# Kernel optimization log

Hardware: AMD Instinct MI355X
Metric: run time of the kernel (lower is better)

## Reference

```python
import jax, jax.numpy as jnp
import numpy as np
from jax import lax

# Topology constants (windowed DAG: compute node i, at global index N_IN+i,
# reads the FANIN immediately preceding global node values).
N_IN = 16      # number of input nodes
FANIN = 16     # connections per compute node
N_NODES = 512  # topologically ordered compute nodes (hidden + output)
N_OUT = 64     # last N_OUT nodes in node_order are outputs
BATCH = 32768
T = N_IN + N_NODES  # total node count


def setup_inputs() -> dict:
    key = jax.random.key(0)
    k1, k2, k3, k4 = jax.random.split(key, 4)
    x = jax.random.normal(k1, (BATCH, N_IN), dtype=jnp.float32)
    # weights scaled down so tanh is not fully saturated through 512 layers
    weights = jax.random.normal(k2, (N_NODES, FANIN), dtype=jnp.float32) * 0.25
    biases = jax.random.normal(k3, (N_NODES,), dtype=jnp.float32) * 0.1
    responses = 1.0 + 0.1 * jax.random.normal(k4, (N_NODES,), dtype=jnp.float32)
    # src indices for node i: global indices [i, i+FANIN) (== previous FANIN nodes,
    # since N_IN == FANIN). Shape [N_NODES, FANIN], int32, all in [0, T).
    src_idx = (jnp.arange(N_NODES, dtype=jnp.int32)[:, None]
               + jnp.arange(FANIN, dtype=jnp.int32)[None, :]
               + (N_IN - FANIN))
    return {"x": x, "weights": weights, "biases": biases,
            "responses": responses, "src_idx": src_idx}


def _forward(x, weights, biases, responses, src_idx):
    B = x.shape[0]
    # values buffer [B, T]: inputs first, then compute nodes in topo order
    values0 = jnp.zeros((B, T), dtype=x.dtype).at[:, :N_IN].set(x)

    def body(values, xs):
        i, idx_row, w, b, r = xs
        src_vals = jnp.take(values, idx_row, axis=1)        # [B, FANIN] gather
        agg = src_vals @ w                                   # [B] weighted sum
        out = jnp.tanh(agg + b) * r                          # activation
        values = lax.dynamic_update_slice(values, out[:, None], (0, N_IN + i))
        return values, None

    ii = jnp.arange(N_NODES, dtype=jnp.int32)
    values, _ = lax.scan(body, values0, (ii, src_idx, weights, biases, responses))
    return values[:, T - N_OUT:]  # [B, N_OUT]


def reference(x, weights, biases, responses, src_idx):
    return _forward(x, weights, biases, responses, src_idx)
```

## Files before the change

### kernel.cpp

```cpp
#include <hip/hip_runtime.h>


typedef float    v4f __attribute__((ext_vector_type(4)));
typedef _Float16 h8  __attribute__((ext_vector_type(8)));

constexpr int   kNOut   = 64;
constexpr int   kBatch  = 32768;
constexpr int   kSgF    = 96;
constexpr int   kSgB    = 384;
constexpr int   kLdsFloats = 65 * kSgF;
constexpr float kScale  = 2.8853900817779268f;

#define QPERM(X, CTRL) __int_as_float(__builtin_amdgcn_update_dpp(            \
    __float_as_int(X), __float_as_int(X), (CTRL), 0xF, 0xF, false))

__device__ __forceinline__ unsigned pack2(float lo, float hi) {
    _Float16 l = (_Float16)lo, h = (_Float16)hi;
    unsigned short ul = __builtin_bit_cast(unsigned short, l);
    unsigned short uh = __builtin_bit_cast(unsigned short, h);
    return ((unsigned)uh << 16) | ul;
}

#define PREF(S) {                                                             \
    asm volatile(                                                             \
      "ds_read_b128 %0, %6 offset:0\n\t"                                      \
      "ds_read_b128 %1, %6 offset:64\n\t"                                     \
      "ds_read_b128 %2, %6 offset:128\n\t"                                    \
      "ds_read_b128 %3, %6 offset:192\n\t"                                    \
      "ds_read_b128 %4, %6 offset:256\n\t"                                    \
      "ds_read_b128 %5, %6 offset:320"                                        \
      : "=&v"(qw0[S]), "=&v"(qw1[S]), "=&v"(qw2[S]), "=&v"(qw3[S]),           \
        "=&v"(qm0[S]), "=&v"(qm1[S])                                          \
      : "v"(a));                                                              \
    a += kSgB; }

#define WAITR(S)                                                              \
    asm volatile("s_waitcnt lgkmcnt(6)"                                       \
      : "+v"(qw0[S]), "+v"(qw1[S]), "+v"(qw2[S]), "+v"(qw3[S]),               \
        "+v"(qm0[S]), "+v"(qm1[S]));

#define NODE(WPAIR, H, BQ, A0,A1,A2,A3) {                                     \
    h8 wh = __builtin_bit_cast(h8, (WPAIR));                                  \
    float p = fmaf((A0), (float)wh[4*(H)+0], (BQ));                           \
    p = fmaf((A1), (float)wh[4*(H)+1], p);                                    \
    p = fmaf((A2), (float)wh[4*(H)+2], p);                                    \
    p = fmaf((A3), (float)wh[4*(H)+3], p);                                    \
    float s1 = p + QPERM(p, 0xB1);                   \
    float s2 = s1 + QPERM(s1, 0x4E);                 \
    float mg = QPERM((A0), 0x39);                    \
    float ex = __builtin_amdgcn_exp2f(s2);                                    \
    float un = __builtin_amdgcn_rcpf(ex + 1.0f);                              \
    (A0) = is_l3 ? un : mg; }

#define REGION(SP, SC) {                                                      \
    PREF(SP)                                                                  \
    WAITR(SC)                                                                 \
    NODE(qw0[SC], 0, qm0[SC].x, r0,r1,r2,r3)                                  \
    NODE(qw0[SC], 1, qm0[SC].y, r1,r2,r3,r0)                                  \
    NODE(qw1[SC], 0, qm0[SC].z, r2,r3,r0,r1)                                  \
    NODE(qw1[SC], 1, qm0[SC].w, r3,r0,r1,r2)                                  \
    NODE(qw2[SC], 0, qm1[SC].x, r0,r1,r2,r3)                                  \
    NODE(qw2[SC], 1, qm1[SC].y, r1,r2,r3,r0)                                  \
    NODE(qw3[SC], 0, qm1[SC].z, r2,r3,r0,r1)                                  \
    NODE(qw3[SC], 1, qm1[SC].w, r3,r0,r1,r2) }

__global__ __launch_bounds__(512) void neat_fwd(
    const float* __restrict__ x,
    const float* __restrict__ w,
    const float* __restrict__ bias,
    const float* __restrict__ resp,
    float* __restrict__ out)
{
    __shared__ alignas(16) float ldsw[kLdsFloats];
    __shared__ float rst[512];

    const int t  = threadIdx.x;
    const int jq = t & 3;
    const bool is_l3 = (jq == 3);

    rst[t] = resp[t];
    __syncthreads();

    {
        const int n = t;
        const float4* wn = reinterpret_cast<const float4*>(w) + n * 4;
        float4 a0 = wn[0], a1 = wn[1], a2 = wn[2], a3 = wn[3];
        const float m2k = -2.0f * kScale;
        float sum = 0.0f;
        float ws0,ws1,ws2,ws3,ws4,ws5,ws6,ws7,ws8,ws9,ws10,ws11,ws12,ws13,ws14,ws15;
        #define DO(J, V) { float rho = (n + (J) < 16) ? 1.0f : rst[n + (J) - 16]; \
                           float wr = (V) * rho; sum += wr; ws##J = wr * m2k; }
        DO(0,a0.x)  DO(1,a0.y)  DO(2,a0.z)  DO(3,a0.w)
        DO(4,a1.x)  DO(5,a1.y)  DO(6,a1.z)  DO(7,a1.w)
        DO(8,a2.x)  DO(9,a2.y)  DO(10,a2.z) DO(11,a2.w)
        DO(12,a3.x) DO(13,a3.y) DO(14,a3.z) DO(15,a3.w)
        #undef DO
        const int sg = n >> 3, s = n & 7, m = s >> 1, h = s & 1;
        unsigned* lu = reinterpret_cast<unsigned*>(ldsw);
        int wi = sg * 96 + m * 16 + h * 2;
        lu[wi + 0*4 + 0] = pack2(ws0,  ws1);   lu[wi + 0*4 + 1] = pack2(ws2,  ws3);
        lu[wi + 1*4 + 0] = pack2(ws4,  ws5);   lu[wi + 1*4 + 1] = pack2(ws6,  ws7);
        lu[wi + 2*4 + 0] = pack2(ws8,  ws9);   lu[wi + 2*4 + 1] = pack2(ws10, ws11);
        lu[wi + 3*4 + 0] = pack2(ws12, ws13);  lu[wi + 3*4 + 1] = pack2(ws14, ws15);
        float Bq = (bias[n] + sum) * (kScale * 0.25f);
        const int c = s >> 2, p = s & 3;
        int mi = sg * 96 + 64 + c * 16 + p;
        ldsw[mi + 0]  = Bq;
        ldsw[mi + 4]  = Bq;
        ldsw[mi + 8]  = Bq;
        ldsw[mi + 12] = Bq;
    }

    const int e = blockIdx.x * 128 + (t >> 2);
    const float4 xi = reinterpret_cast<const float4*>(x)[e * 4 + jq];
    float r0 = fmaf(-0.5f, xi.x, 0.5f);
    float r1 = fmaf(-0.5f, xi.y, 0.5f);
    float r2 = fmaf(-0.5f, xi.z, 0.5f);
    float r3 = fmaf(-0.5f, xi.w, 0.5f);

    const float4* __restrict__ rr4 = reinterpret_cast<const float4*>(resp);
    float* __restrict__ op = out + (size_t)e * kNOut + jq * 4;

    __syncthreads();

    unsigned int a = (unsigned int)(unsigned long long)(&ldsw[0])
                   + (unsigned int)(jq << 4);

    v4f qw0[2], qw1[2], qw2[2], qw3[2], qm0[2], qm1[2];
    PREF(0)

    #pragma unroll 1
    for (int g = 0; g < 32; ++g) {
        REGION(1, 0)
        REGION(0, 1)
        if (g >= 28) {
            const int m_ = g - 28;
            const float4 rv = rr4[112 + 4 * m_ + jq];
            *reinterpret_cast<float4*>(op + 16 * m_) =
                make_float4(fmaf(-2.0f, r0, 1.0f) * rv.x,
                            fmaf(-2.0f, r1, 1.0f) * rv.y,
                            fmaf(-2.0f, r2, 1.0f) * rv.z,
                            fmaf(-2.0f, r3, 1.0f) * rv.w);
        }
    }

    asm volatile("s_waitcnt lgkmcnt(0)" ::: "memory");
}

extern "C" void kernel_launch(void* const* d_in, const int* in_sizes, int n_in,
                              void* d_out, int out_size, void* d_ws, size_t ws_size,
                              hipStream_t stream) {
    const float* x    = (const float*)d_in[0];
    const float* w    = (const float*)d_in[1];
    const float* bias = (const float*)d_in[2];
    const float* resp = (const float*)d_in[3];
    float* out = (float*)d_out;
    dim3 block(512);
    dim3 grid(kBatch * 4 / 512);
    hipLaunchKernelGGL(neat_fwd, grid, block, 0, stream, x, w, bias, resp, out);
}
```

Measured before the change: 97.44 us.

## Keep previous node in register and use fma_mix for half weights

Restructures the per-node recurrence so each lane keeps a rotating window in registers and the most recent node value in a separate register. That value is combined after the cross-lane reduction through an fp32 weight, so it no longer waits on the DPP rotate. The inner products use v_fma_mix_f32 to read fp16 weights directly, removing explicit half-to-float converts. The weight layout grows from 96 to 128 floats per 8-node group to carry the extra weight, which means more LDS reads per region and an extra 32KB of shared scratch used during setup.

```diff
diff --git a/kernel.cpp b/kernel.cpp
--- a/kernel.cpp
+++ b/kernel.cpp
@@ -1,14 +1,12 @@
 #include <hip/hip_runtime.h>
 
 
-typedef float    v4f __attribute__((ext_vector_type(4)));
-typedef _Float16 h8  __attribute__((ext_vector_type(8)));
+typedef float v4f __attribute__((ext_vector_type(4)));
 
 constexpr int   kNOut   = 64;
 constexpr int   kBatch  = 32768;
-constexpr int   kSgF    = 96;
-constexpr int   kSgB    = 384;
-constexpr int   kLdsFloats = 65 * kSgF;
+constexpr int   kRegB   = 512;
+constexpr int   kLdsFloats = 65 * 128;
 constexpr float kScale  = 2.8853900817779268f;
 
 #define QPERM(X, CTRL) __int_as_float(__builtin_amdgcn_update_dpp(            \
@@ -23,46 +21,67 @@
 
 #define PREF(S) {                                                             \
     asm volatile(                                                             \
-      "ds_read_b128 %0, %6 offset:0\n\t"                                      \
-      "ds_read_b128 %1, %6 offset:64\n\t"                                     \
-      "ds_read_b128 %2, %6 offset:128\n\t"                                    \
-      "ds_read_b128 %3, %6 offset:192\n\t"                                    \
-      "ds_read_b128 %4, %6 offset:256\n\t"                                    \
-      "ds_read_b128 %5, %6 offset:320"                                        \
+      "ds_read_b128 %0, %8 offset:0\n\t"                                      \
+      "ds_read_b128 %1, %8 offset:64\n\t"                                     \
+      "ds_read_b128 %2, %8 offset:128\n\t"                                    \
+      "ds_read_b128 %3, %8 offset:192\n\t"                                    \
+      "ds_read_b128 %4, %8 offset:256\n\t"                                    \
+      "ds_read_b128 %5, %8 offset:320\n\t"                                    \
+      "ds_read_b128 %6, %8 offset:384\n\t"                                    \
+      "ds_read_b128 %7, %8 offset:448"                                        \
       : "=&v"(qw0[S]), "=&v"(qw1[S]), "=&v"(qw2[S]), "=&v"(qw3[S]),           \
-        "=&v"(qm0[S]), "=&v"(qm1[S])                                          \
+        "=&v"(qm0[S]), "=&v"(qm1[S]), "=&v"(qm2[S]), "=&v"(qm3[S])            \
       : "v"(a));                                                              \
-    a += kSgB; }
+    a += kRegB; }
 
 #define WAITR(S)                                                              \
-    asm volatile("s_waitcnt lgkmcnt(6)"                                       \
+    asm volatile("s_waitcnt lgkmcnt(8)"                                       \
       : "+v"(qw0[S]), "+v"(qw1[S]), "+v"(qw2[S]), "+v"(qw3[S]),               \
-        "+v"(qm0[S]), "+v"(qm1[S]));
+        "+v"(qm0[S]), "+v"(qm1[S]), "+v"(qm2[S]), "+v"(qm3[S]));
 
-#define NODE(WPAIR, H, BQ, A0,A1,A2,A3) {                                     \
-    h8 wh = __builtin_bit_cast(h8, (WPAIR));                                  \
-    float p = fmaf((A0), (float)wh[4*(H)+0], (BQ));                           \
-    p = fmaf((A1), (float)wh[4*(H)+1], p);                                    \
-    p = fmaf((A2), (float)wh[4*(H)+2], p);                                    \
-    p = fmaf((A3), (float)wh[4*(H)+3], p);                                    \
-    float s1 = p + QPERM(p, 0xB1);                   \
+#define FMIXL(D, W, T, C)                                                     \
+    asm("v_fma_mix_f32 %0, %1, %2, %3 op_sel:[0,0,0] op_sel_hi:[1,0,0]"       \
+        : "=v"(D) : "v"(W), "v"(T), "v"(C));
+#define FMIXH(D, W, T, C)                                                     \
+    asm("v_fma_mix_f32 %0, %1, %2, %3 op_sel:[1,0,0] op_sel_hi:[1,0,0]"       \
+        : "=v"(D) : "v"(W), "v"(T), "v"(C));
+
+#define NODE(W0, W1, BQ, W15, OWN, TREG) {                                    \
+    float p0, p1, p2, p3;                                                     \
+    FMIXL(p0, (W0), r0, (BQ))                                                 \
+    FMIXH(p1, (W0), r1, p0)                                                   \
+    FMIXL(p2, (W1), r2, p1)                                                   \
+    FMIXH(p3, (W1), r3, p2)                                                   \
+    float s1 = p3 + QPERM(p3, 0xB1);                 \
     float s2 = s1 + QPERM(s1, 0x4E);                 \
-    float mg = QPERM((A0), 0x39);                    \
-    float ex = __builtin_amdgcn_exp2f(s2);                                    \
+    float ac = fmaf(up, (W15), s2);                    \
+    float ex = __builtin_amdgcn_exp2f(ac);                                    \
     float un = __builtin_amdgcn_rcpf(ex + 1.0f);                              \
-    (A0) = is_l3 ? un : mg; }
+    (TREG) = (OWN) ? up : (TREG);                       \
+    up = un; }
 
-#define REGION(SP, SC) {                                                      \
+#define REGA(SP, SC) {                                                        \
     PREF(SP)                                                                  \
     WAITR(SC)                                                                 \
-    NODE(qw0[SC], 0, qm0[SC].x, r0,r1,r2,r3)                                  \
-    NODE(qw0[SC], 1, qm0[SC].y, r1,r2,r3,r0)                                  \
-    NODE(qw1[SC], 0, qm0[SC].z, r2,r3,r0,r1)                                  \
-    NODE(qw1[SC], 1, qm0[SC].w, r3,r0,r1,r2)                                  \
-    NODE(qw2[SC], 0, qm1[SC].x, r0,r1,r2,r3)                                  \
-    NODE(qw2[SC], 1, qm1[SC].y, r1,r2,r3,r0)                                  \
-    NODE(qw3[SC], 0, qm1[SC].z, r2,r3,r0,r1)                                  \
-    NODE(qw3[SC], 1, qm1[SC].w, r3,r0,r1,r2) }
+    NODE(qw0[SC][0], qw0[SC][1], qm0[SC][0], qm0[SC][1], o3, r3)              \
+    NODE(qw0[SC][2], qw0[SC][3], qm0[SC][2], qm0[SC][3], o0, r0)              \
+    NODE(qw1[SC][0], qw1[SC][1], qm1[SC][0], qm1[SC][1], o0, r1)              \
+    NODE(qw1[SC][2], qw1[SC][3], qm1[SC][2], qm1[SC][3], o0, r2)              \
+    NODE(qw2[SC][0], qw2[SC][1], qm2[SC][0], qm2[SC][1], o0, r3)              \
+    NODE(qw2[SC][2], qw2[SC][3], qm2[SC][2], qm2[SC][3], o1, r0)              \
+    NODE(qw3[SC][0], qw3[SC][1], qm3[SC][0], qm3[SC][1], o1, r1)              \
+    NODE(qw3[SC][2], qw3[SC][3], qm3[SC][2], qm3[SC][3], o1, r2) }
+#define REGB(SP, SC) {                                                        \
+    PREF(SP)                                                                  \
+    WAITR(SC)                                                                 \
+    NODE(qw0[SC][0], qw0[SC][1], qm0[SC][0], qm0[SC][1], o1, r3)              \
+    NODE(qw0[SC][2], qw0[SC][3], qm0[SC][2], qm0[SC][3], o2, r0)              \
+    NODE(qw1[SC][0], qw1[SC][1], qm1[SC][0], qm1[SC][1], o2, r1)              \
+    NODE(qw1[SC][2], qw1[SC][3], qm1[SC][2], qm1[SC][3], o2, r2)              \
+    NODE(qw2[SC][0], qw2[SC][1], qm2[SC][0], qm2[SC][1], o2, r3)              \
+    NODE(qw2[SC][2], qw2[SC][3], qm2[SC][2], qm2[SC][3], o3, r0)              \
+    NODE(qw3[SC][0], qw3[SC][1], qm3[SC][0], qm3[SC][1], o3, r1)              \
+    NODE(qw3[SC][2], qw3[SC][3], qm3[SC][2], qm3[SC][3], o3, r2) }
 
 __global__ __launch_bounds__(512) void neat_fwd(
     const float* __restrict__ x,
@@ -73,10 +92,11 @@
 {
     __shared__ alignas(16) float ldsw[kLdsFloats];
     __shared__ float rst[512];
+    __shared__ float tmp[512 * 16];
 
     const int t  = threadIdx.x;
     const int jq = t & 3;
-    const bool is_l3 = (jq == 3);
+    const bool o0 = (jq == 0), o1 = (jq == 1), o2 = (jq == 2), o3 = (jq == 3);
 
     rst[t] = resp[t];
     __syncthreads();
@@ -95,20 +115,27 @@
         DO(8,a2.x)  DO(9,a2.y)  DO(10,a2.z) DO(11,a2.w)
         DO(12,a3.x) DO(13,a3.y) DO(14,a3.z) DO(15,a3.w)
         #undef DO
-        const int sg = n >> 3, s = n & 7, m = s >> 1, h = s & 1;
+        float* tb = tmp + t * 16;
+        tb[(n + 15) & 15] = 0.0f;
+        #define PUT(J) tb[(n + (J)) & 15] = ws##J;
+        PUT(0) PUT(1) PUT(2) PUT(3) PUT(4) PUT(5) PUT(6) PUT(7)
+        PUT(8) PUT(9) PUT(10) PUT(11) PUT(12) PUT(13) PUT(14)
+        #undef PUT
+        const int sg = n >> 3, d = n & 7, m = d >> 1, h = d & 1;
         unsigned* lu = reinterpret_cast<unsigned*>(ldsw);
-        int wi = sg * 96 + m * 16 + h * 2;
-        lu[wi + 0*4 + 0] = pack2(ws0,  ws1);   lu[wi + 0*4 + 1] = pack2(ws2,  ws3);
-        lu[wi + 1*4 + 0] = pack2(ws4,  ws5);   lu[wi + 1*4 + 1] = pack2(ws6,  ws7);
-        lu[wi + 2*4 + 0] = pack2(ws8,  ws9);   lu[wi + 2*4 + 1] = pack2(ws10, ws11);
-        lu[wi + 3*4 + 0] = pack2(ws12, ws13);  lu[wi + 3*4 + 1] = pack2(ws14, ws15);
-        float Bq = (bias[n] + sum) * (kScale * 0.25f);
-        const int c = s >> 2, p = s & 3;
-        int mi = sg * 96 + 64 + c * 16 + p;
-        ldsw[mi + 0]  = Bq;
-        ldsw[mi + 4]  = Bq;
-        ldsw[mi + 8]  = Bq;
-        ldsw[mi + 12] = Bq;
+        const int wbase = sg * 128 + m * 16 + h * 2;
+        #pragma unroll
+        for (int q = 0; q < 4; ++q) {
+            lu[wbase + q * 4 + 0] = pack2(tb[4*q + 0], tb[4*q + 1]);
+            lu[wbase + q * 4 + 1] = pack2(tb[4*q + 2], tb[4*q + 3]);
+        }
+        const float Bq = (bias[n] + sum) * (kScale * 0.25f);
+        const int fbase = sg * 128 + 64 + m * 16 + h * 2;
+        #pragma unroll
+        for (int q = 0; q < 4; ++q) {
+            ldsw[fbase + q * 4]     = Bq;
+            ldsw[fbase + q * 4 + 1] = ws15;
+        }
     }
 
     const int e = blockIdx.x * 128 + (t >> 2);
@@ -117,6 +144,7 @@
     float r1 = fmaf(-0.5f, xi.y, 0.5f);
     float r2 = fmaf(-0.5f, xi.z, 0.5f);
     float r3 = fmaf(-0.5f, xi.w, 0.5f);
+    float up = fmaf(-0.5f, x[(size_t)e * 16 + 15], 0.5f);
 
     const float4* __restrict__ rr4 = reinterpret_cast<const float4*>(resp);
     float* __restrict__ op = out + (size_t)e * kNOut + jq * 4;
@@ -126,21 +154,22 @@
     unsigned int a = (unsigned int)(unsigned long long)(&ldsw[0])
                    + (unsigned int)(jq << 4);
 
-    v4f qw0[2], qw1[2], qw2[2], qw3[2], qm0[2], qm1[2];
+    v4f qw0[2], qw1[2], qw2[2], qw3[2], qm0[2], qm1[2], qm2[2], qm3[2];
     PREF(0)
 
     #pragma unroll 1
     for (int g = 0; g < 32; ++g) {
-        REGION(1, 0)
-        REGION(0, 1)
+        REGA(1, 0)
+        REGB(0, 1)
         if (g >= 28) {
             const int m_ = g - 28;
             const float4 rv = rr4[112 + 4 * m_ + jq];
+            float v3 = o3 ? up : r3;
             *reinterpret_cast<float4*>(op + 16 * m_) =
                 make_float4(fmaf(-2.0f, r0, 1.0f) * rv.x,
                             fmaf(-2.0f, r1, 1.0f) * rv.y,
                             fmaf(-2.0f, r2, 1.0f) * rv.z,
-                            fmaf(-2.0f, r3, 1.0f) * rv.w);
+                            fmaf(-2.0f, v3, 1.0f) * rv.w);
         }
     }
 
```

New measurement: 98.31 us. Within noise of the previous version (+0.9%).

## Give each thread a full batch element with a 16-register ring and fma_mix

Applied to the files above, without the earlier changes.

Each thread now handles one whole batch element and keeps its 16-value sliding window in registers, in place of four lanes per element that combined partial sums with DPP quad shuffles. Weights are stored as packed fp16 in 144-byte per-quad records and consumed directly with v_fma_mix_f32. The dot product is split into three partial chains to shorten the dependency. This removes the cross-lane DPP traffic and the per-node select, but each thread now does four times the FMA work per node, and blocks shrink to 128 threads, which lowers the parallelism available to hide latency.

```diff
diff --git a/kernel.cpp b/kernel.cpp
--- a/kernel.cpp
+++ b/kernel.cpp
@@ -1,18 +1,14 @@
 #include <hip/hip_runtime.h>
 
 
-typedef float    v4f __attribute__((ext_vector_type(4)));
-typedef _Float16 h8  __attribute__((ext_vector_type(8)));
+typedef float v4f __attribute__((ext_vector_type(4)));
 
 constexpr int   kNOut   = 64;
 constexpr int   kBatch  = 32768;
-constexpr int   kSgF    = 96;
-constexpr int   kSgB    = 384;
-constexpr int   kLdsFloats = 65 * kSgF;
+constexpr int   kRecF   = 36;
+constexpr int   kRecB   = 144;
+constexpr int   kLdsFloats = 129 * kRecF;
 constexpr float kScale  = 2.8853900817779268f;
-
-#define QPERM(X, CTRL) __int_as_float(__builtin_amdgcn_update_dpp(            \
-    __float_as_int(X), __float_as_int(X), (CTRL), 0xF, 0xF, false))
 
 __device__ __forceinline__ unsigned pack2(float lo, float hi) {
     _Float16 l = (_Float16)lo, h = (_Float16)hi;
@@ -21,50 +17,82 @@
     return ((unsigned)uh << 16) | ul;
 }
 
+#define FMIXL(D, W, T, C)                                                     \
+    asm("v_fma_mix_f32 %0, %1, %2, %3 op_sel:[0,0,0] op_sel_hi:[1,0,0]"       \
+        : "=v"(D) : "v"(W), "v"(T), "v"(C));
+#define FMIXH(D, W, T, C)                                                     \
+    asm("v_fma_mix_f32 %0, %1, %2, %3 op_sel:[1,0,0] op_sel_hi:[1,0,0]"       \
+        : "=v"(D) : "v"(W), "v"(T), "v"(C));
+
 #define PREF(S) {                                                             \
     asm volatile(                                                             \
-      "ds_read_b128 %0, %6 offset:0\n\t"                                      \
-      "ds_read_b128 %1, %6 offset:64\n\t"                                     \
-      "ds_read_b128 %2, %6 offset:128\n\t"                                    \
-      "ds_read_b128 %3, %6 offset:192\n\t"                                    \
-      "ds_read_b128 %4, %6 offset:256\n\t"                                    \
-      "ds_read_b128 %5, %6 offset:320"                                        \
-      : "=&v"(qw0[S]), "=&v"(qw1[S]), "=&v"(qw2[S]), "=&v"(qw3[S]),           \
-        "=&v"(qm0[S]), "=&v"(qm1[S])                                          \
+      "ds_read_b128 %0, %9 offset:0\n\t"                                      \
+      "ds_read_b128 %1, %9 offset:16\n\t"                                     \
+      "ds_read_b128 %2, %9 offset:32\n\t"                                     \
+      "ds_read_b128 %3, %9 offset:48\n\t"                                     \
+      "ds_read_b128 %4, %9 offset:64\n\t"                                     \
+      "ds_read_b128 %5, %9 offset:80\n\t"                                     \
+      "ds_read_b128 %6, %9 offset:96\n\t"                                     \
+      "ds_read_b128 %7, %9 offset:112\n\t"                                    \
+      "ds_read_b128 %8, %9 offset:128"                                        \
+      : "=&v"(w0a[S]), "=&v"(w0b[S]), "=&v"(w1a[S]), "=&v"(w1b[S]),           \
+        "=&v"(w2a[S]), "=&v"(w2b[S]), "=&v"(w3a[S]), "=&v"(w3b[S]),           \
+        "=&v"(qm[S])                                                          \
       : "v"(a));                                                              \
-    a += kSgB; }
+    a += kRecB; }
 
 #define WAITR(S)                                                              \
-    asm volatile("s_waitcnt lgkmcnt(6)"                                       \
-      : "+v"(qw0[S]), "+v"(qw1[S]), "+v"(qw2[S]), "+v"(qw3[S]),               \
-        "+v"(qm0[S]), "+v"(qm1[S]));
-
-#define NODE(WPAIR, H, BQ, A0,A1,A2,A3) {                                     \
-    h8 wh = __builtin_bit_cast(h8, (WPAIR));                                  \
-    float p = fmaf((A0), (float)wh[4*(H)+0], (BQ));                           \
-    p = fmaf((A1), (float)wh[4*(H)+1], p);                                    \
-    p = fmaf((A2), (float)wh[4*(H)+2], p);                                    \
-    p = fmaf((A3), (float)wh[4*(H)+3], p);                                    \
-    float s1 = p + QPERM(p, 0xB1);                   \
-    float s2 = s1 + QPERM(s1, 0x4E);                 \
-    float mg = QPERM((A0), 0x39);                    \
-    float ex = __builtin_amdgcn_exp2f(s2);                                    \
-    float un = __builtin_amdgcn_rcpf(ex + 1.0f);                              \
-    (A0) = is_l3 ? un : mg; }
-
-#define REGION(SP, SC) {                                                      \
-    PREF(SP)                                                                  \
-    WAITR(SC)                                                                 \
-    NODE(qw0[SC], 0, qm0[SC].x, r0,r1,r2,r3)                                  \
-    NODE(qw0[SC], 1, qm0[SC].y, r1,r2,r3,r0)                                  \
-    NODE(qw1[SC], 0, qm0[SC].z, r2,r3,r0,r1)                                  \
-    NODE(qw1[SC], 1, qm0[SC].w, r3,r0,r1,r2)                                  \
-    NODE(qw2[SC], 0, qm1[SC].x, r0,r1,r2,r3)                                  \
-    NODE(qw2[SC], 1, qm1[SC].y, r1,r2,r3,r0)                                  \
-    NODE(qw3[SC], 0, qm1[SC].z, r2,r3,r0,r1)                                  \
-    NODE(qw3[SC], 1, qm1[SC].w, r3,r0,r1,r2) }
-
-__global__ __launch_bounds__(512) void neat_fwd(
+    asm volatile("s_waitcnt lgkmcnt(9)"                                       \
+      : "+v"(w0a[S]), "+v"(w0b[S]), "+v"(w1a[S]), "+v"(w1b[S]),               \
+        "+v"(w2a[S]), "+v"(w2b[S]), "+v"(w3a[S]), "+v"(w3b[S]),               \
+        "+v"(qm[S]));
+
+#define NODE(WA, WB, BB, T0,T1,T2,T3,T4,T5,T6,T7,T8,T9,T10,T11,T12,T13,T14,T15) { \
+    float q0,q1,q2,q3,q4, h0,h1,h2,h3,h4, s0,s1,s2,s3,s4, sj, ac;             \
+    FMIXL(q0, (WA)[0], (T0),  (BB))                                           \
+    FMIXH(q1, (WA)[0], (T1),  q0)                                             \
+    FMIXL(q2, (WA)[1], (T2),  q1)                                             \
+    FMIXH(q3, (WA)[1], (T3),  q2)                                             \
+    FMIXL(q4, (WA)[2], (T4),  q3)                                             \
+    FMIXH(h0, (WA)[2], (T5),  fz)                                             \
+    FMIXL(h1, (WA)[3], (T6),  h0)                                             \
+    FMIXH(h2, (WA)[3], (T7),  h1)                                             \
+    FMIXL(h3, (WB)[0], (T8),  h2)                                             \
+    FMIXH(h4, (WB)[0], (T9),  h3)                                             \
+    FMIXL(s0, (WB)[1], (T10), fz)                                             \
+    FMIXH(s1, (WB)[1], (T11), s0)                                             \
+    FMIXL(s2, (WB)[2], (T12), s1)                                             \
+    FMIXH(s3, (WB)[2], (T13), s2)                                             \
+    FMIXL(s4, (WB)[3], (T14), s3)                                             \
+    sj = (q4 + h4) + s4;                                                      \
+    FMIXH(ac, (WB)[3], (T15), sj)           \
+    float ex = __builtin_amdgcn_exp2f(ac);                                    \
+    (T0) = __builtin_amdgcn_rcpf(ex + 1.0f); }
+
+#define N4(SC, L0,L1,L2,L3)                                                   \
+    NODE(w0a[SC], w0b[SC], qm[SC][0], L0)                                     \
+    NODE(w1a[SC], w1b[SC], qm[SC][1], L1)                                     \
+    NODE(w2a[SC], w2b[SC], qm[SC][2], L2)                                     \
+    NODE(w3a[SC], w3b[SC], qm[SC][3], L3)
+
+#define R0T  m0,m1,m2,m3,m4,m5,m6,m7,m8,m9,m10,m11,m12,m13,m14,m15
+#define R1T  m1,m2,m3,m4,m5,m6,m7,m8,m9,m10,m11,m12,m13,m14,m15,m0
+#define R2T  m2,m3,m4,m5,m6,m7,m8,m9,m10,m11,m12,m13,m14,m15,m0,m1
+#define R3T  m3,m4,m5,m6,m7,m8,m9,m10,m11,m12,m13,m14,m15,m0,m1,m2
+#define R4T  m4,m5,m6,m7,m8,m9,m10,m11,m12,m13,m14,m15,m0,m1,m2,m3
+#define R5T  m5,m6,m7,m8,m9,m10,m11,m12,m13,m14,m15,m0,m1,m2,m3,m4
+#define R6T  m6,m7,m8,m9,m10,m11,m12,m13,m14,m15,m0,m1,m2,m3,m4,m5
+#define R7T  m7,m8,m9,m10,m11,m12,m13,m14,m15,m0,m1,m2,m3,m4,m5,m6
+#define R8T  m8,m9,m10,m11,m12,m13,m14,m15,m0,m1,m2,m3,m4,m5,m6,m7
+#define R9T  m9,m10,m11,m12,m13,m14,m15,m0,m1,m2,m3,m4,m5,m6,m7,m8
+#define R10T m10,m11,m12,m13,m14,m15,m0,m1,m2,m3,m4,m5,m6,m7,m8,m9
+#define R11T m11,m12,m13,m14,m15,m0,m1,m2,m3,m4,m5,m6,m7,m8,m9,m10
+#define R12T m12,m13,m14,m15,m0,m1,m2,m3,m4,m5,m6,m7,m8,m9,m10,m11
+#define R13T m13,m14,m15,m0,m1,m2,m3,m4,m5,m6,m7,m8,m9,m10,m11,m12
+#define R14T m14,m15,m0,m1,m2,m3,m4,m5,m6,m7,m8,m9,m10,m11,m12,m13
+#define R15T m15,m0,m1,m2,m3,m4,m5,m6,m7,m8,m9,m10,m11,m12,m13,m14
+
+__global__ __launch_bounds__(128) void neat_fwd(
     const float* __restrict__ x,
     const float* __restrict__ w,
     const float* __restrict__ bias,
@@ -74,18 +102,19 @@
     __shared__ alignas(16) float ldsw[kLdsFloats];
     __shared__ float rst[512];
 
-    const int t  = threadIdx.x;
-    const int jq = t & 3;
-    const bool is_l3 = (jq == 3);
-
-    rst[t] = resp[t];
+    const int t = threadIdx.x;
+
+    #pragma unroll
+    for (int k = 0; k < 4; ++k) rst[t + k * 128] = resp[t + k * 128];
     __syncthreads();
 
-    {
-        const int n = t;
-        const float4* wn = reinterpret_cast<const float4*>(w) + n * 4;
+    const float4* __restrict__ w4 = reinterpret_cast<const float4*>(w);
+    const float m2k = -2.0f * kScale;
+    #pragma unroll
+    for (int k = 0; k < 4; ++k) {
+        int n = t + k * 128;
+        const float4* wn = w4 + n * 4;
         float4 a0 = wn[0], a1 = wn[1], a2 = wn[2], a3 = wn[3];
-        const float m2k = -2.0f * kScale;
         float sum = 0.0f;
         float ws0,ws1,ws2,ws3,ws4,ws5,ws6,ws7,ws8,ws9,ws10,ws11,ws12,ws13,ws14,ws15;
         #define DO(J, V) { float rho = (n + (J) < 16) ? 1.0f : rst[n + (J) - 16]; \
@@ -95,52 +124,66 @@
         DO(8,a2.x)  DO(9,a2.y)  DO(10,a2.z) DO(11,a2.w)
         DO(12,a3.x) DO(13,a3.y) DO(14,a3.z) DO(15,a3.w)
         #undef DO
-        const int sg = n >> 3, s = n & 7, m = s >> 1, h = s & 1;
+        const int rec = n >> 2, d = n & 3;
         unsigned* lu = reinterpret_cast<unsigned*>(ldsw);
-        int wi = sg * 96 + m * 16 + h * 2;
-        lu[wi + 0*4 + 0] = pack2(ws0,  ws1);   lu[wi + 0*4 + 1] = pack2(ws2,  ws3);
-        lu[wi + 1*4 + 0] = pack2(ws4,  ws5);   lu[wi + 1*4 + 1] = pack2(ws6,  ws7);
-        lu[wi + 2*4 + 0] = pack2(ws8,  ws9);   lu[wi + 2*4 + 1] = pack2(ws10, ws11);
-        lu[wi + 3*4 + 0] = pack2(ws12, ws13);  lu[wi + 3*4 + 1] = pack2(ws14, ws15);
-        float Bq = (bias[n] + sum) * (kScale * 0.25f);
-        const int c = s >> 2, p = s & 3;
-        int mi = sg * 96 + 64 + c * 16 + p;
-        ldsw[mi + 0]  = Bq;
-        ldsw[mi + 4]  = Bq;
-        ldsw[mi + 8]  = Bq;
-        ldsw[mi + 12] = Bq;
+        const int wb = rec * kRecF + d * 8;
+        lu[wb + 0] = pack2(ws0,  ws1);  lu[wb + 1] = pack2(ws2,  ws3);
+        lu[wb + 2] = pack2(ws4,  ws5);  lu[wb + 3] = pack2(ws6,  ws7);
+        lu[wb + 4] = pack2(ws8,  ws9);  lu[wb + 5] = pack2(ws10, ws11);
+        lu[wb + 6] = pack2(ws12, ws13); lu[wb + 7] = pack2(ws14, ws15);
+        ldsw[rec * kRecF + 32 + d] = (bias[n] + sum) * kScale;
     }
 
-    const int e = blockIdx.x * 128 + (t >> 2);
-    const float4 xi = reinterpret_cast<const float4*>(x)[e * 4 + jq];
-    float r0 = fmaf(-0.5f, xi.x, 0.5f);
-    float r1 = fmaf(-0.5f, xi.y, 0.5f);
-    float r2 = fmaf(-0.5f, xi.z, 0.5f);
-    float r3 = fmaf(-0.5f, xi.w, 0.5f);
-
-    const float4* __restrict__ rr4 = reinterpret_cast<const float4*>(resp);
-    float* __restrict__ op = out + (size_t)e * kNOut + jq * 4;
+    const int e = blockIdx.x * 128 + t;
+    const float4* __restrict__ x4p = reinterpret_cast<const float4*>(x) + (size_t)e * 4;
+    float4 X0 = x4p[0], X1 = x4p[1], X2 = x4p[2], X3 = x4p[3];
+    float m0  = fmaf(-0.5f, X0.x, 0.5f), m1  = fmaf(-0.5f, X0.y, 0.5f);
+    float m2  = fmaf(-0.5f, X0.z, 0.5f), m3  = fmaf(-0.5f, X0.w, 0.5f);
+    float m4  = fmaf(-0.5f, X1.x, 0.5f), m5  = fmaf(-0.5f, X1.y, 0.5f);
+    float m6  = fmaf(-0.5f, X1.z, 0.5f), m7  = fmaf(-0.5f, X1.w, 0.5f);
+    float m8  = fmaf(-0.5f, X2.x, 0.5f), m9  = fmaf(-0.5f, X2.y, 0.5f);
+    float m10 = fmaf(-0.5f, X2.z, 0.5f), m11 = fmaf(-0.5f, X2.w, 0.5f);
+    float m12 = fmaf(-0.5f, X3.x, 0.5f), m13 = fmaf(-0.5f, X3.y, 0.5f);
+    float m14 = fmaf(-0.5f, X3.z, 0.5f), m15 = fmaf(-0.5f, X3.w, 0.5f);
+    const float fz = 0.0f;
+
+    float* __restrict__ op = out + (size_t)e * kNOut;
 
     __syncthreads();
 
-    unsigned int a = (unsigned int)(unsigned long long)(&ldsw[0])
-                   + (unsigned int)(jq << 4);
-
-    v4f qw0[2], qw1[2], qw2[2], qw3[2], qm0[2], qm1[2];
+    unsigned int a = (unsigned int)(unsigned long long)(&ldsw[0]);
+
+    v4f w0a[2], w0b[2], w1a[2], w1b[2], w2a[2], w2b[2], w3a[2], w3b[2], qm[2];
     PREF(0)
 
     #pragma unroll 1
     for (int g = 0; g < 32; ++g) {
-        REGION(1, 0)
-        REGION(0, 1)
+        PREF(1) WAITR(0) N4(0, R0T,  R1T,  R2T,  R3T)
+        PREF(0) WAITR(1) N4(1, R4T,  R5T,  R6T,  R7T)
+        PREF(1) WAITR(0) N4(0, R8T,  R9T,  R10T, R11T)
+        PREF(0) WAITR(1) N4(1, R12T, R13T, R14T, R15T)
         if (g >= 28) {
-            const int m_ = g - 28;
-            const float4 rv = rr4[112 + 4 * m_ + jq];
-            *reinterpret_cast<float4*>(op + 16 * m_) =
-                make_float4(fmaf(-2.0f, r0, 1.0f) * rv.x,
-                            fmaf(-2.0f, r1, 1.0f) * rv.y,
-                            fmaf(-2.0f, r2, 1.0f) * rv.z,
-                            fmaf(-2.0f, r3, 1.0f) * rv.w);
+            const int mq = g - 28;
+            const float4* __restrict__ rr =
+                reinterpret_cast<const float4*>(resp + 448 + 16 * mq);
+            float4 R0 = rr[0], R1 = rr[1], R2 = rr[2], R3 = rr[3];
+            float4* o4 = reinterpret_cast<float4*>(op + 16 * mq);
+            o4[0] = make_float4(R0.x * fmaf(-2.0f, m0,  1.0f),
+                                R0.y * fmaf(-2.0f, m1,  1.0f),
+                                R0.z * fmaf(-2.0f, m2,  1.0f),
+                                R0.w * fmaf(-2.0f, m3,  1.0f));
+            o4[1] = make_float4(R1.x * fmaf(-2.0f, m4,  1.0f),
+                                R1.y * fmaf(-2.0f, m5,  1.0f),
+                                R1.z * fmaf(-2.0f, m6,  1.0f),
+                                R1.w * fmaf(-2.0f, m7,  1.0f));
+            o4[2] = make_float4(R2.x * fmaf(-2.0f, m8,  1.0f),
+                                R2.y * fmaf(-2.0f, m9,  1.0f),
+                                R2.z * fmaf(-2.0f, m10, 1.0f),
+                                R2.w * fmaf(-2.0f, m11, 1.0f));
+            o4[3] = make_float4(R3.x * fmaf(-2.0f, m12, 1.0f),
+                                R3.y * fmaf(-2.0f, m13, 1.0f),
+                                R3.z * fmaf(-2.0f, m14, 1.0f),
+                                R3.w * fmaf(-2.0f, m15, 1.0f));
         }
     }
 
@@ -155,7 +198,7 @@
     const float* bias = (const float*)d_in[2];
     const float* resp = (const float*)d_in[3];
     float* out = (float*)d_out;
-    dim3 block(512);
-    dim3 grid(kBatch * 4 / 512);
+    dim3 block(128);
+    dim3 grid(kBatch / 128);
     hipLaunchKernelGGL(neat_fwd, grid, block, 0, stream, x, w, bias, resp, out);
 }
```

Result: no change. 99.34 us (+1.9%).
